# Optimization experiments

Hardware: AMD Instinct MI355X
Metric: run time of the kernel (lower is better)

Reference implementation:

```python
import jax, jax.numpy as jnp
import numpy as np


def setup_inputs() -> dict:
    key = jax.random.key(0)
    kq, kk, kv = jax.random.split(key, 3)
    B, S, H, D = 2, 2048, 32, 128
    q = jax.random.normal(kq, (B, S, H, D), dtype=jnp.float32)
    k = jax.random.normal(kk, (B, S, H, D), dtype=jnp.float32)
    v = jax.random.normal(kv, (B, S, H, D), dtype=jnp.float32)
    return {"q": q, "k": k, "v": v}


def _causal_attention(q, k, v):
    # q,k,v: [B, S, H, D] (flash-attn layout). Zigzag ring attention computes
    # exactly standard causal attention; zigzag only balances work across ranks.
    B, S, H, D = q.shape
    scale = 1.0 / jnp.sqrt(jnp.asarray(D, q.dtype))
    scores = jnp.einsum('bqhd,bkhd->bhqk', q, k) * scale  # [B,H,S,S]
    causal = jnp.tril(jnp.ones((S, S), dtype=bool))
    scores = jnp.where(causal, scores, jnp.finfo(scores.dtype).min)
    probs = jax.nn.softmax(scores, axis=-1)
    return jnp.einsum('bhqk,bkhd->bqhd', probs, v)  # [B,S,H,D]


def reference(q, k, v):
    out = _causal_attention(q, k, v)
    return jnp.sum(out)
```

## Files before the change

kernel.cpp:

```cpp
#include <hip/hip_runtime.h>
#include <hip/hip_bf16.h>
#include <stdint.h>

#define B_ 2
#define S_ 2048
#define H_ 32
#define D_ 128
#define R_ (B_*H_*S_)
#define PG 2048
#define CPB 27

typedef __bf16 bf16x8 __attribute__((ext_vector_type(8)));
typedef float  f32x16 __attribute__((ext_vector_type(16)));

#if __has_builtin(__builtin_amdgcn_exp2f)
#define EXP2F(x) __builtin_amdgcn_exp2f(x)
#else
#define EXP2F(x) exp2f(x)
#endif

#define AS1 __attribute__((address_space(1)))
#define AS3 __attribute__((address_space(3)))

__device__ __forceinline__ unsigned short f2bf(float f) {
  unsigned u = __float_as_uint(f);
  u += 0x7FFFu + ((u >> 16) & 1u);
  return (unsigned short)(u >> 16);
}

__device__ __forceinline__ unsigned int cvtpk(float a, float b) {
  unsigned int r;
  asm("v_cvt_pk_bf16_f32 %0, %1, %2" : "=v"(r) : "v"(a), "v"(b));
  return r;
}

__global__ __launch_bounds__(256) void prep(
    const float* __restrict__ kf, const float* __restrict__ v,
    unsigned short* __restrict__ kc,
    float* __restrict__ vsum, float* __restrict__ nd, float* __restrict__ out0) {
  const int bid = blockIdx.x;
  const int t = threadIdx.x;
  if (bid == 0 && t == 0) out0[0] = 0.f;

  #pragma unroll
  for (int g = 0; g < 4; ++g) {
    const size_t i = (size_t)g * (PG * 256) + (size_t)bid * 256 + t;
    const float4 a = *reinterpret_cast<const float4*>(kf + i * 8);
    const float4 b = *reinterpret_cast<const float4*>(kf + i * 8 + 4);
    union { unsigned short u[8]; uint4 v4; } o;
    o.u[0] = f2bf(a.x); o.u[1] = f2bf(a.y);
    o.u[2] = f2bf(a.z); o.u[3] = f2bf(a.w);
    o.u[4] = f2bf(b.x); o.u[5] = f2bf(b.y);
    o.u[6] = f2bf(b.z); o.u[7] = f2bf(b.w);
    *reinterpret_cast<uint4*>(kc + i * 8) = o.v4;
  }

  #pragma unroll
  for (int g = 0; g < (B_ * S_) / PG; ++g) {
    const int u = bid + g * PG;
    const int b = u / S_, s = u % S_;
    const float4* panel =
        reinterpret_cast<const float4*>(v + (((size_t)b * S_ + s) * H_) * D_);
    #pragma unroll
    for (int j = 0; j < 4; ++j) {
      const float4 a = panel[j * 256 + t];
      float sum = a.x + a.y + a.z + a.w;
      sum += __shfl_xor(sum, 1);
      sum += __shfl_xor(sum, 2);
      sum += __shfl_xor(sum, 4);
      sum += __shfl_xor(sum, 8);
      sum += __shfl_xor(sum, 16);
      const int h = j * 8 + (t >> 5);
      if ((t & 31) == 0) vsum[((size_t)b * H_ + h) * S_ + s] = sum;
    }
  }

  if (bid < 256) {
    float4* p = reinterpret_cast<float4*>(nd);
    p[(size_t)bid * 256 + t] = float4{0.f, 0.f, 0.f, 0.f};
  }
}

__global__ __launch_bounds__(256, 3) void attn_sum(
    const float* __restrict__ qf, const unsigned short* __restrict__ kc,
    const float* __restrict__ vsum, float* __restrict__ numb,
    float* __restrict__ denb) {
  __shared__ uint4 kbuf[3][512];
  __shared__ float vsbuf[3][64];

  const int id = blockIdx.x;
  const int y  = id >> 3;
  const int bh = (id & 7) + 8 * (y / CPB);
  const int c  = y % CPB;

  int g, h, nch;
  if (c < 1)       { g = 0; h = c;      nch = 1; }
  else if (c < 3)  { g = 1; h = c - 1;  nch = 2; }
  else if (c < 5)  { g = 2; h = c - 3;  nch = 2; }
  else if (c < 8)  { g = 3; h = c - 5;  nch = 3; }
  else if (c < 12) { g = 4; h = c - 8;  nch = 4; }
  else if (c < 16) { g = 5; h = c - 12; nch = 4; }
  else if (c < 21) { g = 6; h = c - 16; nch = 5; }
  else             { g = 7; h = c - 21; nch = 6; }
  const int nkt  = 4 * g + 4;
  const int bas_ = nkt / nch, rem = nkt % nch;
  const int kt0  = h * bas_ + (h < rem ? h : rem);
  const int kt1  = kt0 + bas_ + (h < rem ? 1 : 0);
  const int st0  = 2 * kt0, st1 = 2 * kt1;

  const int t  = threadIdx.x;
  const int w  = t >> 6;
  const int l  = t & 63;
  const int ln = l & 31, l5 = l >> 5;

  const int b0 = bh >> 5, h0 = bh & 31;
  const int qminA = (2 * g) * 128 + w * 32;
  const int qminB = (2 * g + 1) * 128 + w * 32;
  const unsigned short* kc0 = kc + ((size_t)b0 * S_ * H_ + h0) * D_;
  const float* vsrc0 = vsum + (size_t)bh * S_;

  const float sc = 0.0883883476483184f * 1.4426950408889634f;
  bf16x8 qfA[8], qfB[8];
  {
    const float* qpA = qf + (((size_t)b0 * S_ + qminA + ln) * H_ + h0) * D_ + l5 * 8;
    const float* qpB = qf + (((size_t)b0 * S_ + qminB + ln) * H_ + h0) * D_ + l5 * 8;
    #pragma unroll
    for (int kb8 = 0; kb8 < 8; ++kb8) {
      float4 a = *reinterpret_cast<const float4*>(qpA + kb8 * 16);
      float4 b = *reinterpret_cast<const float4*>(qpA + kb8 * 16 + 4);
      union { unsigned int u[4]; bf16x8 v; } oA;
      oA.u[0] = cvtpk(a.x * sc, a.y * sc); oA.u[1] = cvtpk(a.z * sc, a.w * sc);
      oA.u[2] = cvtpk(b.x * sc, b.y * sc); oA.u[3] = cvtpk(b.z * sc, b.w * sc);
      qfA[kb8] = oA.v;
      a = *reinterpret_cast<const float4*>(qpB + kb8 * 16);
      b = *reinterpret_cast<const float4*>(qpB + kb8 * 16 + 4);
      union { unsigned int u[4]; bf16x8 v; } oB;
      oB.u[0] = cvtpk(a.x * sc, a.y * sc); oB.u[1] = cvtpk(a.z * sc, a.w * sc);
      oB.u[2] = cvtpk(b.x * sc, b.y * sc); oB.u[3] = cvtpk(b.z * sc, b.w * sc);
      qfB[kb8] = oB.v;
    }
  }

  auto stage = [&](int st, int slot) {
    #pragma unroll
    for (int j = 0; j < 2; ++j) {
      const int idx = (w * 2 + j) * 64 + l;
      const int r   = idx >> 4;
      const int p   = idx & 15;
      const int cc  = p ^ (r & 15);
      const unsigned short* src = kc0 + (size_t)(st * 32 + r) * (H_ * D_) + cc * 8;
      __builtin_amdgcn_global_load_lds(
          (const AS1 void*)src, (AS3 void*)(&kbuf[slot][idx & ~63]), 16, 0, 0);
    }
    __builtin_amdgcn_global_load_lds(
        (const AS1 void*)(vsrc0 + st * 32 + l), (AS3 void*)(&vsbuf[slot][0]), 4, 0, 0);
  };

  float npA = 0.f, dpA = 0.f, npB = 0.f, dpB = 0.f;

  stage(st0, st0 % 3);
  stage(st0 + 1, (st0 + 1) % 3);

  const int xr = ln & 15;
  for (int st = st0; st < st1; ++st) {
    if (st + 1 < st1) asm volatile("s_waitcnt vmcnt(3)" ::: "memory");
    else              asm volatile("s_waitcnt vmcnt(0)" ::: "memory");
    __builtin_amdgcn_s_barrier();
    if (st + 2 < st1) stage(st + 2, (st + 2) % 3);

    const int kbase = st * 32;
    if (kbase <= qminB + 31) {
      const int slot = st % 3;
      const uint4* rowb = &kbuf[slot][ln * 16];
      bf16x8 kfr[8];
      #pragma unroll
      for (int kb8 = 0; kb8 < 8; ++kb8)
        kfr[kb8] = *reinterpret_cast<const bf16x8*>(&rowb[(kb8 * 2 + l5) ^ xr]);
      const float4 vs0 = *reinterpret_cast<const float4*>(&vsbuf[slot][ 0 + 4 * l5]);
      const float4 vs1 = *reinterpret_cast<const float4*>(&vsbuf[slot][ 8 + 4 * l5]);
      const float4 vs2 = *reinterpret_cast<const float4*>(&vsbuf[slot][16 + 4 * l5]);
      const float4 vs3 = *reinterpret_cast<const float4*>(&vsbuf[slot][24 + 4 * l5]);
      const float vsa[16] = {vs0.x,vs0.y,vs0.z,vs0.w, vs1.x,vs1.y,vs1.z,vs1.w,
                             vs2.x,vs2.y,vs2.z,vs2.w, vs3.x,vs3.y,vs3.z,vs3.w};

      {
        f32x16 sacc = {0.f,0.f,0.f,0.f,0.f,0.f,0.f,0.f,
                       0.f,0.f,0.f,0.f,0.f,0.f,0.f,0.f};
        __builtin_amdgcn_s_setprio(1);
        #pragma unroll
        for (int kb8 = 0; kb8 < 8; ++kb8)
          sacc = __builtin_amdgcn_mfma_f32_32x32x16_bf16(kfr[kb8], qfB[kb8], sacc, 0, 0, 0);
        __builtin_amdgcn_s_setprio(0);
        if (kbase + 31 <= qminB) {
          #pragma unroll
          for (int r = 0; r < 16; ++r) {
            const float e = EXP2F(sacc[r]);
            dpB += e;
            npB = fmaf(e, vsa[r], npB);
          }
        } else {
          const int qg = qminB + ln;
          #pragma unroll
          for (int r = 0; r < 16; ++r) {
            const int kr = kbase + (r & 3) + 8 * (r >> 2) + 4 * l5;
            const float e = (kr <= qg) ? EXP2F(sacc[r]) : 0.f;
            dpB += e;
            npB = fmaf(e, vsa[r], npB);
          }
        }
      }
      if (kbase <= qminA + 31) {
        f32x16 sacc = {0.f,0.f,0.f,0.f,0.f,0.f,0.f,0.f,
                       0.f,0.f,0.f,0.f,0.f,0.f,0.f,0.f};
        __builtin_amdgcn_s_setprio(1);
        #pragma unroll
        for (int kb8 = 0; kb8 < 8; ++kb8)
          sacc = __builtin_amdgcn_mfma_f32_32x32x16_bf16(kfr[kb8], qfA[kb8], sacc, 0, 0, 0);
        __builtin_amdgcn_s_setprio(0);
        if (kbase + 31 <= qminA) {
          #pragma unroll
          for (int r = 0; r < 16; ++r) {
            const float e = EXP2F(sacc[r]);
            dpA += e;
            npA = fmaf(e, vsa[r], npA);
          }
        } else {
          const int qg = qminA + ln;
          #pragma unroll
          for (int r = 0; r < 16; ++r) {
            const int kr = kbase + (r & 3) + 8 * (r >> 2) + 4 * l5;
            const float e = (kr <= qg) ? EXP2F(sacc[r]) : 0.f;
            dpA += e;
            npA = fmaf(e, vsa[r], npA);
          }
        }
      }
    }
  }

  npA += __shfl_xor(npA, 32); dpA += __shfl_xor(dpA, 32);
  npB += __shfl_xor(npB, 32); dpB += __shfl_xor(dpB, 32);
  if (l5 == 0) {
    float* nrow = numb + (size_t)bh * S_;
    float* drow = denb + (size_t)bh * S_;
    atomicAdd(&nrow[qminA + ln], npA);
    atomicAdd(&drow[qminA + ln], dpA);
    atomicAdd(&nrow[qminB + ln], npB);
    atomicAdd(&drow[qminB + ln], dpB);
  }
}

__global__ __launch_bounds__(256) void finalize(
    const float* __restrict__ numb, const float* __restrict__ denb,
    float* __restrict__ out) {
  const int i = blockIdx.x * 256 + threadIdx.x;
  float c = numb[i] / denb[i];
  #pragma unroll
  for (int m = 1; m < 64; m <<= 1) c += __shfl_xor(c, m);
  __shared__ float ps[4];
  if ((threadIdx.x & 63) == 0) ps[threadIdx.x >> 6] = c;
  __syncthreads();
  if (threadIdx.x == 0) atomicAdd(out, ps[0] + ps[1] + ps[2] + ps[3]);
}

extern "C" void kernel_launch(void* const* d_in, const int* in_sizes, int n_in,
                              void* d_out, int out_size, void* d_ws, size_t ws_size,
                              hipStream_t stream) {
  const float* q = (const float*)d_in[0];
  const float* k = (const float*)d_in[1];
  const float* v = (const float*)d_in[2];
  float* out = (float*)d_out;

  unsigned short* kc = (unsigned short*)d_ws;
  float* vsum = (float*)(kc + (size_t)R_ * D_);
  float* numb = vsum + R_;
  float* denb = numb + R_;

  hipLaunchKernelGGL(prep, dim3(PG), dim3(256), 0, stream,
                     k, v, kc, vsum, numb, out);
  hipLaunchKernelGGL(attn_sum, dim3(64 * CPB), dim3(256), 0, stream,
                     q, kc, vsum, numb, denb);
  hipLaunchKernelGGL(finalize, dim3(R_ / 256), dim3(256), 0, stream,
                     numb, denb, out);
}
```

Before: 100.6 us.

## Process four query tiles per block to reuse each staged K tile

Each attention block now holds four 128-row query tiles in registers instead of two, so every K/vsum tile staged into LDS feeds up to four MFMA score passes. The work split changes to uniform 8-stage key chunks, giving 20 chunks per batch-head instead of 27 variable-size ones. The goal is to halve K and vsum traffic and the per-block staging and barrier overhead per unit of compute. In exchange, register use grows and launch bounds drop to 2 waves per SIMD, which lowers occupancy and latency hiding. The grid also has fewer, larger blocks.

```diff
diff --git a/kernel.cpp b/kernel.cpp
--- a/kernel.cpp
+++ b/kernel.cpp
@@ -8,7 +8,7 @@
 #define D_ 128
 #define R_ (B_*H_*S_)
 #define PG 2048
-#define CPB 27
+#define CPB 20
 
 typedef __bf16 bf16x8 __attribute__((ext_vector_type(8)));
 typedef float  f32x16 __attribute__((ext_vector_type(16)));
@@ -81,7 +81,7 @@
   }
 }
 
-__global__ __launch_bounds__(256, 3) void attn_sum(
+__global__ __launch_bounds__(256, 2) void attn_sum(
     const float* __restrict__ qf, const unsigned short* __restrict__ kc,
     const float* __restrict__ vsum, float* __restrict__ numb,
     float* __restrict__ denb) {
@@ -93,20 +93,12 @@
   const int bh = (id & 7) + 8 * (y / CPB);
   const int c  = y % CPB;
 
-  int g, h, nch;
-  if (c < 1)       { g = 0; h = c;      nch = 1; }
-  else if (c < 3)  { g = 1; h = c - 1;  nch = 2; }
-  else if (c < 5)  { g = 2; h = c - 3;  nch = 2; }
-  else if (c < 8)  { g = 3; h = c - 5;  nch = 3; }
-  else if (c < 12) { g = 4; h = c - 8;  nch = 4; }
-  else if (c < 16) { g = 5; h = c - 12; nch = 4; }
-  else if (c < 21) { g = 6; h = c - 16; nch = 5; }
-  else             { g = 7; h = c - 21; nch = 6; }
-  const int nkt  = 4 * g + 4;
-  const int bas_ = nkt / nch, rem = nkt % nch;
-  const int kt0  = h * bas_ + (h < rem ? h : rem);
-  const int kt1  = kt0 + bas_ + (h < rem ? 1 : 0);
-  const int st0  = 2 * kt0, st1 = 2 * kt1;
+  int g, h;
+  if (c < 2)       { g = 0; h = c;      }
+  else if (c < 6)  { g = 1; h = c - 2;  }
+  else if (c < 12) { g = 2; h = c - 6;  }
+  else             { g = 3; h = c - 12; }
+  const int st0 = h * 8, st1 = st0 + 8;
 
   const int t  = threadIdx.x;
   const int w  = t >> 6;
@@ -114,30 +106,24 @@
   const int ln = l & 31, l5 = l >> 5;
 
   const int b0 = bh >> 5, h0 = bh & 31;
-  const int qminA = (2 * g) * 128 + w * 32;
-  const int qminB = (2 * g + 1) * 128 + w * 32;
+  const int qm0 = (4 * g) * 128 + w * 32;
   const unsigned short* kc0 = kc + ((size_t)b0 * S_ * H_ + h0) * D_;
   const float* vsrc0 = vsum + (size_t)bh * S_;
 
   const float sc = 0.0883883476483184f * 1.4426950408889634f;
-  bf16x8 qfA[8], qfB[8];
-  {
-    const float* qpA = qf + (((size_t)b0 * S_ + qminA + ln) * H_ + h0) * D_ + l5 * 8;
-    const float* qpB = qf + (((size_t)b0 * S_ + qminB + ln) * H_ + h0) * D_ + l5 * 8;
+  bf16x8 qf4[4][8];
+  #pragma unroll
+  for (int x = 0; x < 4; ++x) {
+    const float* qp =
+        qf + (((size_t)b0 * S_ + qm0 + x * 128 + ln) * H_ + h0) * D_ + l5 * 8;
     #pragma unroll
     for (int kb8 = 0; kb8 < 8; ++kb8) {
-      float4 a = *reinterpret_cast<const float4*>(qpA + kb8 * 16);
-      float4 b = *reinterpret_cast<const float4*>(qpA + kb8 * 16 + 4);
-      union { unsigned int u[4]; bf16x8 v; } oA;
-      oA.u[0] = cvtpk(a.x * sc, a.y * sc); oA.u[1] = cvtpk(a.z * sc, a.w * sc);
-      oA.u[2] = cvtpk(b.x * sc, b.y * sc); oA.u[3] = cvtpk(b.z * sc, b.w * sc);
-      qfA[kb8] = oA.v;
-      a = *reinterpret_cast<const float4*>(qpB + kb8 * 16);
-      b = *reinterpret_cast<const float4*>(qpB + kb8 * 16 + 4);
-      union { unsigned int u[4]; bf16x8 v; } oB;
-      oB.u[0] = cvtpk(a.x * sc, a.y * sc); oB.u[1] = cvtpk(a.z * sc, a.w * sc);
-      oB.u[2] = cvtpk(b.x * sc, b.y * sc); oB.u[3] = cvtpk(b.z * sc, b.w * sc);
-      qfB[kb8] = oB.v;
+      const float4 a = *reinterpret_cast<const float4*>(qp + kb8 * 16);
+      const float4 b = *reinterpret_cast<const float4*>(qp + kb8 * 16 + 4);
+      union { unsigned int u[4]; bf16x8 v; } o;
+      o.u[0] = cvtpk(a.x * sc, a.y * sc); o.u[1] = cvtpk(a.z * sc, a.w * sc);
+      o.u[2] = cvtpk(b.x * sc, b.y * sc); o.u[3] = cvtpk(b.z * sc, b.w * sc);
+      qf4[x][kb8] = o.v;
     }
   }
 
@@ -156,7 +142,7 @@
         (const AS1 void*)(vsrc0 + st * 32 + l), (AS3 void*)(&vsbuf[slot][0]), 4, 0, 0);
   };
 
-  float npA = 0.f, dpA = 0.f, npB = 0.f, dpB = 0.f;
+  float np[4] = {0.f,0.f,0.f,0.f}, dp[4] = {0.f,0.f,0.f,0.f};
 
   stage(st0, st0 % 3);
   stage(st0 + 1, (st0 + 1) % 3);
@@ -169,84 +155,63 @@
     if (st + 2 < st1) stage(st + 2, (st + 2) % 3);
 
     const int kbase = st * 32;
-    if (kbase <= qminB + 31) {
-      const int slot = st % 3;
-      const uint4* rowb = &kbuf[slot][ln * 16];
-      bf16x8 kfr[8];
+    const int slot = st % 3;
+    const uint4* rowb = &kbuf[slot][ln * 16];
+    bf16x8 kfr[8];
+    #pragma unroll
+    for (int kb8 = 0; kb8 < 8; ++kb8)
+      kfr[kb8] = *reinterpret_cast<const bf16x8*>(&rowb[(kb8 * 2 + l5) ^ xr]);
+    const float4 vs0 = *reinterpret_cast<const float4*>(&vsbuf[slot][ 0 + 4 * l5]);
+    const float4 vs1 = *reinterpret_cast<const float4*>(&vsbuf[slot][ 8 + 4 * l5]);
+    const float4 vs2 = *reinterpret_cast<const float4*>(&vsbuf[slot][16 + 4 * l5]);
+    const float4 vs3 = *reinterpret_cast<const float4*>(&vsbuf[slot][24 + 4 * l5]);
+    const float vsa[16] = {vs0.x,vs0.y,vs0.z,vs0.w, vs1.x,vs1.y,vs1.z,vs1.w,
+                           vs2.x,vs2.y,vs2.z,vs2.w, vs3.x,vs3.y,vs3.z,vs3.w};
+
+    #pragma unroll
+    for (int x = 3; x >= 0; --x) {
+      const int qmin = qm0 + x * 128;
+      if (kbase > qmin + 31) continue;
+      f32x16 sacc = {0.f,0.f,0.f,0.f,0.f,0.f,0.f,0.f,
+                     0.f,0.f,0.f,0.f,0.f,0.f,0.f,0.f};
+      __builtin_amdgcn_s_setprio(1);
       #pragma unroll
       for (int kb8 = 0; kb8 < 8; ++kb8)
-        kfr[kb8] = *reinterpret_cast<const bf16x8*>(&rowb[(kb8 * 2 + l5) ^ xr]);
-      const float4 vs0 = *reinterpret_cast<const float4*>(&vsbuf[slot][ 0 + 4 * l5]);
-      const float4 vs1 = *reinterpret_cast<const float4*>(&vsbuf[slot][ 8 + 4 * l5]);
-      const float4 vs2 = *reinterpret_cast<const float4*>(&vsbuf[slot][16 + 4 * l5]);
-      const float4 vs3 = *reinterpret_cast<const float4*>(&vsbuf[slot][24 + 4 * l5]);
-      const float vsa[16] = {vs0.x,vs0.y,vs0.z,vs0.w, vs1.x,vs1.y,vs1.z,vs1.w,
-                             vs2.x,vs2.y,vs2.z,vs2.w, vs3.x,vs3.y,vs3.z,vs3.w};
-
-      {
-        f32x16 sacc = {0.f,0.f,0.f,0.f,0.f,0.f,0.f,0.f,
-                       0.f,0.f,0.f,0.f,0.f,0.f,0.f,0.f};
-        __builtin_amdgcn_s_setprio(1);
+        sacc = __builtin_amdgcn_mfma_f32_32x32x16_bf16(kfr[kb8], qf4[x][kb8], sacc, 0, 0, 0);
+      __builtin_amdgcn_s_setprio(0);
+      if (kbase + 31 <= qmin) {
         #pragma unroll
-        for (int kb8 = 0; kb8 < 8; ++kb8)
-          sacc = __builtin_amdgcn_mfma_f32_32x32x16_bf16(kfr[kb8], qfB[kb8], sacc, 0, 0, 0);
-        __builtin_amdgcn_s_setprio(0);
-        if (kbase + 31 <= qminB) {
-          #pragma unroll
-          for (int r = 0; r < 16; ++r) {
-            const float e = EXP2F(sacc[r]);
-            dpB += e;
-            npB = fmaf(e, vsa[r], npB);
-          }
-        } else {
-          const int qg = qminB + ln;
-          #pragma unroll
-          for (int r = 0; r < 16; ++r) {
-            const int kr = kbase + (r & 3) + 8 * (r >> 2) + 4 * l5;
-            const float e = (kr <= qg) ? EXP2F(sacc[r]) : 0.f;
-            dpB += e;
-            npB = fmaf(e, vsa[r], npB);
-          }
+        for (int r = 0; r < 16; ++r) {
+          const float e = EXP2F(sacc[r]);
+          dp[x] += e;
+          np[x] = fmaf(e, vsa[r], np[x]);
+        }
+      } else {
+        const int qg = qmin + ln;
+        #pragma unroll
+        for (int r = 0; r < 16; ++r) {
+          const int kr = kbase + (r & 3) + 8 * (r >> 2) + 4 * l5;
+          const float e = (kr <= qg) ? EXP2F(sacc[r]) : 0.f;
+          dp[x] += e;
+          np[x] = fmaf(e, vsa[r], np[x]);
         }
       }
-      if (kbase <= qminA + 31) {
-        f32x16 sacc = {0.f,0.f,0.f,0.f,0.f,0.f,0.f,0.f,
-                       0.f,0.f,0.f,0.f,0.f,0.f,0.f,0.f};
-        __builtin_amdgcn_s_setprio(1);
-        #pragma unroll
-        for (int kb8 = 0; kb8 < 8; ++kb8)
-          sacc = __builtin_amdgcn_mfma_f32_32x32x16_bf16(kfr[kb8], qfA[kb8], sacc, 0, 0, 0);
-        __builtin_amdgcn_s_setprio(0);
-        if (kbase + 31 <= qminA) {
-          #pragma unroll
-          for (int r = 0; r < 16; ++r) {
-            const float e = EXP2F(sacc[r]);
-            dpA += e;
-            npA = fmaf(e, vsa[r], npA);
-          }
-        } else {
-          const int qg = qminA + ln;
-          #pragma unroll
-          for (int r = 0; r < 16; ++r) {
-            const int kr = kbase + (r & 3) + 8 * (r >> 2) + 4 * l5;
-            const float e = (kr <= qg) ? EXP2F(sacc[r]) : 0.f;
-            dpA += e;
-            npA = fmaf(e, vsa[r], npA);
-          }
-        }
-      }
-    }
-  }
-
-  npA += __shfl_xor(npA, 32); dpA += __shfl_xor(dpA, 32);
-  npB += __shfl_xor(npB, 32); dpB += __shfl_xor(dpB, 32);
+    }
+  }
+
+  #pragma unroll
+  for (int x = 0; x < 4; ++x) {
+    np[x] += __shfl_xor(np[x], 32);
+    dp[x] += __shfl_xor(dp[x], 32);
+  }
   if (l5 == 0) {
     float* nrow = numb + (size_t)bh * S_;
     float* drow = denb + (size_t)bh * S_;
-    atomicAdd(&nrow[qminA + ln], npA);
-    atomicAdd(&drow[qminA + ln], dpA);
-    atomicAdd(&nrow[qminB + ln], npB);
-    atomicAdd(&drow[qminB + ln], dpB);
+    #pragma unroll
+    for (int x = 0; x < 4; ++x) {
+      atomicAdd(&nrow[qm0 + x * 128 + ln], np[x]);
+      atomicAdd(&drow[qm0 + x * 128 + ln], dp[x]);
+    }
   }
 }
 
```

Result: slower. 111.0 us (+10.3%).
